# Kernel optimization log

Measured on AMD Instinct MI355X. Metric: run time of the kernel, lower is better.

## Reference

```python
import jax, jax.numpy as jnp
import numpy as np

KSZ = 3      # kernel_size
NH = 4       # num_heads


def setup_inputs() -> dict:
    key = jax.random.key(0)
    ks = jax.random.split(key, 4)
    B, D, H, W, C = 1, 28, 28, 28, 192
    N = D * H * W
    s = 0.02  # trunc_normal std used by the module's init
    return {
        "x": jax.random.normal(ks[0], (B, N, C), jnp.float32),
        "Wq": jax.random.normal(ks[1], (C, C), jnp.float32) * s,
        "bq": jnp.zeros((C,), jnp.float32),
        "Wkv": jax.random.normal(ks[2], (C, 2 * C), jnp.float32) * s,
        "bkv": jnp.zeros((2 * C,), jnp.float32),
        "Wp": jax.random.normal(ks[3], (C, C), jnp.float32) * s,
        "bp": jnp.zeros((C,), jnp.float32),
        "D": D, "H": H, "W": W,
    }


def _windows(t, D, H, W):
    # t: (B, D+2, H+2, W+2, nh, hc) zero-padded; gather the 27 neighborhood
    # offsets (same flattening order as unfold: d-major, then h, then w).
    return jnp.stack(
        [t[:, dz:dz + D, dy:dy + H, dx:dx + W]
         for dz in range(KSZ) for dy in range(KSZ) for dx in range(KSZ)],
        axis=4)  # (B, D, H, W, 27, nh, hc)


def reference(x, Wq, bq, Wkv, bkv, Wp, bp, D, H, W):
    B, N, C = x.shape
    hc = C // NH
    scale = hc ** (-0.5)
    xv = x.reshape(B, D, H, W, C)

    q = (xv @ Wq + bq).reshape(B, D, H, W, NH, hc) * scale
    kv = (xv @ Wkv + bkv).reshape(B, D, H, W, 2, NH, hc)
    k, v = kv[..., 0, :, :], kv[..., 1, :, :]

    pad = ((0, 0), (1, 1), (1, 1), (1, 1), (0, 0), (0, 0))
    kwin = _windows(jnp.pad(k, pad), D, H, W)  # (B,D,H,W,27,nh,hc)
    vwin = _windows(jnp.pad(v, pad), D, H, W)

    # per-voxel 1x27 attention over the 3x3x3 neighborhood
    attn = jnp.einsum('bdhwnc,bdhwknc->bdhwnk', q, kwin)
    attn = jax.nn.softmax(attn, axis=-1)
    out = jnp.einsum('bdhwnk,bdhwknc->bdhwnc', attn, vwin)
    out = out.reshape(B, D, H, W, C) @ Wp + bp
    return out.reshape(B, N, C)
```

## Files before the change

kernel.cpp:

```cpp
#include <hip/hip_runtime.h>
#include <hip/hip_bf16.h>
#include <math.h>

#define CDIM 192
#define DD 28
#define NVOX (DD * DD * DD)
#define NLINE (DD * DD)
#define LSTRIDE (24 * DD * 8)

typedef __attribute__((ext_vector_type(8))) short bf16x8;
typedef __attribute__((ext_vector_type(4))) float f32x4;

__device__ __forceinline__ float blo(unsigned int u) {
  union { unsigned int i; float f; } w; w.i = u << 16; return w.f;
}
__device__ __forceinline__ float bhi(unsigned int u) {
  union { unsigned int i; float f; } w; w.i = u & 0xffff0000u; return w.f;
}
__device__ __forceinline__ unsigned short f2bf(float f) {
  union { float ff; unsigned int i; } w; w.ff = f;
  unsigned int x = w.i;
  return (unsigned short)((x + 0x7fffu + ((x >> 16) & 1u)) >> 16);
}
__device__ __forceinline__ unsigned int pk2(float lo, float hi) {
  __hip_bfloat162 h = __float22bfloat162_rn(make_float2(lo, hi));
  union { __hip_bfloat162 h2; unsigned int u; } cv; cv.h2 = h; return cv.u;
}

__global__ __launch_bounds__(256) void prep_w(
    const float* __restrict__ Wq, const float* __restrict__ Wkv,
    const float* __restrict__ Wp, const float* __restrict__ bq,
    const float* __restrict__ bkv,
    unsigned short* __restrict__ WqkvT, unsigned short* __restrict__ WpT,
    float* __restrict__ biasAll, float scale)
{
  int t = blockIdx.x * 256 + threadIdx.x;
  if (t < 576 * CDIM) {
    const int n = t / CDIM, k = t % CDIM;
    const float v = (n < CDIM) ? Wq[k * CDIM + n] * scale
                               : Wkv[k * 2 * CDIM + (n - CDIM)];
    WqkvT[t] = f2bf(v);
    return;
  }
  t -= 576 * CDIM;
  if (t < CDIM * CDIM) {
    const int n = t / CDIM, k = t % CDIM;
    WpT[t] = f2bf(Wp[k * CDIM + n]);
    return;
  }
  t -= CDIM * CDIM;
  if (t < 576)
    biasAll[t] = (t < CDIM) ? bq[t] * scale : bkv[t - CDIM];
}

__global__ __launch_bounds__(256) void gemm_qkv(
    const float* __restrict__ X,
    const unsigned short* __restrict__ Bt,
    const float* __restrict__ biasAll,
    unsigned short* __restrict__ qb,
    unsigned short* __restrict__ kxb,
    unsigned short* __restrict__ vxb)
{
  __shared__ unsigned short As[64 * 200];
  __shared__ unsigned short Bs[64 * 200];
  const int tid = threadIdx.x;
  const int m0 = blockIdx.x * 64;
  const int by = blockIdx.y;

#pragma unroll
  for (int u = tid; u < 1536; u += 256) {
    const int row = u / 24, c = (u % 24) * 8;
    const float4 f0 = *(const float4*)(&X[(size_t)(m0 + row) * CDIM + c]);
    const float4 f1 = *(const float4*)(&X[(size_t)(m0 + row) * CDIM + c + 4]);
    unsigned int o[4] = {pk2(f0.x, f0.y), pk2(f0.z, f0.w),
                         pk2(f1.x, f1.y), pk2(f1.z, f1.w)};
    *(uint4*)(&As[row * 200 + c]) = *(const uint4*)o;
  }

  const int l = tid & 63, w = tid >> 6;
  const int wm = (w >> 1) * 32, wn = (w & 1) * 32;
  const int lr = l & 15, lk = (l >> 4) * 8;
  const unsigned short* pa = &As[(wm + lr) * 200 + lk];
  const unsigned short* pb = &Bs[(wn + lr) * 200 + lk];

  for (int nt = by; nt < 9; nt += 3) {
    const int n0 = nt * 64;
    __syncthreads();
#pragma unroll
    for (int u = tid; u < 1536; u += 256) {
      const int row = u / 24, c = (u % 24) * 8;
      *(uint4*)(&Bs[row * 200 + c]) =
          *(const uint4*)(&Bt[(size_t)(n0 + row) * CDIM + c]);
    }
    __syncthreads();

    f32x4 acc[2][2] = {};
#pragma unroll
    for (int k0 = 0; k0 < CDIM; k0 += 32) {
      const bf16x8 a0 = *(const bf16x8*)(pa + k0);
      const bf16x8 a1 = *(const bf16x8*)(pa + 16 * 200 + k0);
      const bf16x8 b0 = *(const bf16x8*)(pb + k0);
      const bf16x8 b1 = *(const bf16x8*)(pb + 16 * 200 + k0);
      acc[0][0] = __builtin_amdgcn_mfma_f32_16x16x32_bf16(a0, b0, acc[0][0], 0, 0, 0);
      acc[0][1] = __builtin_amdgcn_mfma_f32_16x16x32_bf16(a0, b1, acc[0][1], 0, 0, 0);
      acc[1][0] = __builtin_amdgcn_mfma_f32_16x16x32_bf16(a1, b0, acc[1][0], 0, 0, 0);
      acc[1][1] = __builtin_amdgcn_mfma_f32_16x16x32_bf16(a1, b1, acc[1][1], 0, 0, 0);
    }

#pragma unroll
    for (int i = 0; i < 2; ++i)
#pragma unroll
      for (int j = 0; j < 2; ++j) {
        const int gc = n0 + wn + j * 16 + lr;
        const float bv = biasAll[gc];
#pragma unroll
        for (int r = 0; r < 4; ++r) {
          const int gr = m0 + wm + i * 16 + (l >> 4) * 4 + r;
          const float v = acc[i][j][r] + bv;
          const unsigned short bfv = f2bf(v);
          if (gc < CDIM) {
            qb[(size_t)gr * CDIM + gc] = bfv;
          } else {
            const int cc = (gc < 2 * CDIM) ? gc - CDIM : gc - 2 * CDIM;
            const int zy = gr / DD, xx = gr - zy * DD;
            const int dst = zy * LSTRIDE + (cc >> 3) * (DD * 8) + xx * 8 + (cc & 7);
            if (gc < 2 * CDIM) kxb[dst] = bfv;
            else               vxb[dst] = bfv;
          }
        }
      }
  }
}

__global__ __launch_bounds__(256, 3) void attn3d_proj(
    const unsigned short* __restrict__ q,
    const unsigned short* __restrict__ kx,
    const unsigned short* __restrict__ vx,
    const unsigned short* __restrict__ WpT,
    const float* __restrict__ bp,
    float* __restrict__ C)
{
  __shared__ unsigned short ytile[32 * 200];

  const int bid = blockIdx.x;
  const int zy = (bid & 7) * 98 + (bid >> 3);
  const int z = zy / 28, yr = zy % 28;
  const int h = threadIdx.x >> 6;
  const int lane = threadIdx.x & 63;
  const int x = lane & 31;
  const int xc = x < 28 ? x : 27;
  const int g = lane >> 5;
  const int cb = h * 48 + g * 24;
  const int cgb = h * 6 + g * 3;
  const int vox = zy * 28 + xc;

  if (threadIdx.x < 100)
    *(uint4*)(&ytile[28 * 200 + threadIdx.x * 8]) = make_uint4(0, 0, 0, 0);

  float qf[24];
  {
    const uint4* qp = (const uint4*)(q + (size_t)vox * CDIM + cb);
    const uint4 a = qp[0], b = qp[1], c = qp[2];
    const unsigned int uu[12] = {a.x, a.y, a.z, a.w, b.x, b.y, b.z, b.w,
                                 c.x, c.y, c.z, c.w};
#pragma unroll
    for (int i = 0; i < 12; ++i) { qf[2*i] = blo(uu[i]); qf[2*i+1] = bhi(uu[i]); }
  }

  const int nx = 3 - (x == 0) - (x == 27);
  const int ny = 3 - (yr == 0) - (yr == 27);
  const int nz = 3 - (z == 0) - (z == 27);
  const int noob = 27 - nx * ny * nz;
  float m = noob ? 0.f : -INFINITY;
  float s = (float)noob;
  float out[24];
#pragma unroll
  for (int i = 0; i < 24; ++i) out[i] = 0.f;

  const bool okm = (x > 0), okp = (x < 27);
  const int xm = okm ? xc - 1 : 0;
  const int xp = okp ? xc + 1 : 27;

  int offm[3], offc[3], offp[3];
#pragma unroll
  for (int i = 0; i < 3; ++i) {
    const int ub = (cgb + i) * (DD * 8);
    offm[i] = ub + xm * 8; offc[i] = ub + xc * 8; offp[i] = ub + xp * 8;
  }

  for (int dz = -1; dz <= 1; ++dz) {
    const int zz = z + dz;
    if ((unsigned)zz >= 28u) continue;
    for (int dy = -1; dy <= 1; ++dy) {
      const int yv = yr + dy;
      if ((unsigned)yv >= 28u) continue;
      const size_t lbase = (size_t)(zz * 28 + yv) * LSTRIDE;
      const unsigned short* kl = kx + lbase;
      const unsigned short* vl = vx + lbase;

      const uint4 Km0 = *(const uint4*)(kl + offm[0]);
      const uint4 Km1 = *(const uint4*)(kl + offm[1]);
      const uint4 Km2 = *(const uint4*)(kl + offm[2]);
      const uint4 Kc0 = *(const uint4*)(kl + offc[0]);
      const uint4 Kc1 = *(const uint4*)(kl + offc[1]);
      const uint4 Kc2 = *(const uint4*)(kl + offc[2]);
      const uint4 Kp0 = *(const uint4*)(kl + offp[0]);
      const uint4 Kp1 = *(const uint4*)(kl + offp[1]);
      const uint4 Kp2 = *(const uint4*)(kl + offp[2]);
      const unsigned int km[12] = {Km0.x, Km0.y, Km0.z, Km0.w, Km1.x, Km1.y,
                                   Km1.z, Km1.w, Km2.x, Km2.y, Km2.z, Km2.w};
      const unsigned int kc[12] = {Kc0.x, Kc0.y, Kc0.z, Kc0.w, Kc1.x, Kc1.y,
                                   Kc1.z, Kc1.w, Kc2.x, Kc2.y, Kc2.z, Kc2.w};
      const unsigned int kp[12] = {Kp0.x, Kp0.y, Kp0.z, Kp0.w, Kp1.x, Kp1.y,
                                   Kp1.z, Kp1.w, Kp2.x, Kp2.y, Kp2.z, Kp2.w};
      float p0 = 0.f, p1 = 0.f, p2 = 0.f;
#pragma unroll
      for (int i = 0; i < 12; ++i) {
        p0 += qf[2*i] * blo(km[i]) + qf[2*i+1] * bhi(km[i]);
        p1 += qf[2*i] * blo(kc[i]) + qf[2*i+1] * bhi(kc[i]);
        p2 += qf[2*i] * blo(kp[i]) + qf[2*i+1] * bhi(kp[i]);
      }
      p0 += __shfl_xor(p0, 32);
      p1 += __shfl_xor(p1, 32);
      p2 += __shfl_xor(p2, 32);

      const uint4 Vm0 = *(const uint4*)(vl + offm[0]);
      const uint4 Vm1 = *(const uint4*)(vl + offm[1]);
      const uint4 Vm2 = *(const uint4*)(vl + offm[2]);
      const uint4 Vc0 = *(const uint4*)(vl + offc[0]);
      const uint4 Vc1 = *(const uint4*)(vl + offc[1]);
      const uint4 Vc2 = *(const uint4*)(vl + offc[2]);
      const uint4 Vp0 = *(const uint4*)(vl + offp[0]);
      const uint4 Vp1 = *(const uint4*)(vl + offp[1]);
      const uint4 Vp2 = *(const uint4*)(vl + offp[2]);

      const float l0 = okm ? p0 : -INFINITY;
      const float l2 = okp ? p2 : -INFINITY;
      const float nm = fmaxf(m, fmaxf(p1, fmaxf(l0, l2)));
      const float sc = __expf(m - nm);
      const float w0 = okm ? __expf(p0 - nm) : 0.f;
      const float w1 = __expf(p1 - nm);
      const float w2 = okp ? __expf(p2 - nm) : 0.f;
      s = s * sc + w0 + w1 + w2;
      m = nm;

      const unsigned int vm[12] = {Vm0.x, Vm0.y, Vm0.z, Vm0.w, Vm1.x, Vm1.y,
                                   Vm1.z, Vm1.w, Vm2.x, Vm2.y, Vm2.z, Vm2.w};
      const unsigned int vc[12] = {Vc0.x, Vc0.y, Vc0.z, Vc0.w, Vc1.x, Vc1.y,
                                   Vc1.z, Vc1.w, Vc2.x, Vc2.y, Vc2.z, Vc2.w};
      const unsigned int vp[12] = {Vp0.x, Vp0.y, Vp0.z, Vp0.w, Vp1.x, Vp1.y,
                                   Vp1.z, Vp1.w, Vp2.x, Vp2.y, Vp2.z, Vp2.w};
#pragma unroll
      for (int i = 0; i < 12; ++i) {
        out[2*i]   = out[2*i]   * sc + w0 * blo(vm[i]) + w1 * blo(vc[i]) + w2 * blo(vp[i]);
        out[2*i+1] = out[2*i+1] * sc + w0 * bhi(vm[i]) + w1 * bhi(vc[i]) + w2 * bhi(vp[i]);
      }
    }
  }

  if (x < 28) {
    const float inv = 1.f / s;
    unsigned int ou[12];
#pragma unroll
    for (int i = 0; i < 12; ++i)
      ou[i] = pk2(out[2*i] * inv, out[2*i+1] * inv);
    uint4* yp = (uint4*)(&ytile[xc * 200 + cb]);
    yp[0] = make_uint4(ou[0], ou[1], ou[2], ou[3]);
    yp[1] = make_uint4(ou[4], ou[5], ou[6], ou[7]);
    yp[2] = make_uint4(ou[8], ou[9], ou[10], ou[11]);
  }
  __syncthreads();

  const int w = threadIdx.x >> 6;
  const int lr = lane & 15, lk = (lane >> 4) * 8;
  const int nb = w * 48;

  f32x4 acc[2][3] = {};
#pragma unroll
  for (int k0 = 0; k0 < CDIM; k0 += 32) {
    const bf16x8 a0 = *(const bf16x8*)(&ytile[(0 + lr) * 200 + lk + k0]);
    const bf16x8 a1 = *(const bf16x8*)(&ytile[(16 + lr) * 200 + lk + k0]);
#pragma unroll
    for (int nj = 0; nj < 3; ++nj) {
      const bf16x8 b = *(const bf16x8*)(
          &WpT[(size_t)(nb + nj * 16 + lr) * CDIM + lk + k0]);
      acc[0][nj] = __builtin_amdgcn_mfma_f32_16x16x32_bf16(a0, b, acc[0][nj], 0, 0, 0);
      acc[1][nj] = __builtin_amdgcn_mfma_f32_16x16x32_bf16(a1, b, acc[1][nj], 0, 0, 0);
    }
  }

#pragma unroll
  for (int nj = 0; nj < 3; ++nj) {
    const int gc = nb + nj * 16 + lr;
    const float bv = bp[gc];
#pragma unroll
    for (int mi = 0; mi < 2; ++mi)
#pragma unroll
      for (int r = 0; r < 4; ++r) {
        const int row = mi * 16 + (lane >> 4) * 4 + r;
        if (row < 28)
          C[(size_t)(zy * 28 + row) * CDIM + gc] = acc[mi][nj][r] + bv;
      }
  }
}

extern "C" void kernel_launch(void* const* d_in, const int* in_sizes, int n_in,
                              void* d_out, int out_size, void* d_ws, size_t ws_size,
                              hipStream_t stream) {
  const float* x   = (const float*)d_in[0];
  const float* Wq  = (const float*)d_in[1];
  const float* bq  = (const float*)d_in[2];
  const float* Wkv = (const float*)d_in[3];
  const float* bkv = (const float*)d_in[4];
  const float* Wp  = (const float*)d_in[5];
  const float* bp  = (const float*)d_in[6];
  float* out = (float*)d_out;

  unsigned short* WqkvT = (unsigned short*)d_ws;
  unsigned short* WpT   = WqkvT + 576 * CDIM;
  float*          biasA = (float*)(WpT + CDIM * CDIM);
  unsigned short* qb    = (unsigned short*)(biasA + 576);
  unsigned short* kxb   = qb + (size_t)NVOX * CDIM;
  unsigned short* vxb   = kxb + (size_t)NLINE * LSTRIDE;

  const float scale = 1.0f / sqrtf(48.0f);

  prep_w<<<(148032 + 255) / 256, 256, 0, stream>>>(
      Wq, Wkv, Wp, bq, bkv, WqkvT, WpT, biasA, scale);

  gemm_qkv<<<dim3(NVOX / 64, 3), 256, 0, stream>>>(x, WqkvT, biasA, qb, kxb, vxb);
  attn3d_proj<<<NLINE, 256, 0, stream>>>(qb, kxb, vxb, WpT, bp, out);
}
```

Before: 144.6 us.

## Pre-pack weights into MFMA fragment order and compute QKV per line

Weights are pre-packed so each lane's MFMA B-fragment is one contiguous 16-byte global load, with no shared-memory staging of B. The QKV GEMM now runs one block per 28-voxel line that computes all 576 output columns, reading X once instead of once per column group. The projection in the attention kernel uses the same packed layout. Per-wave register pressure rises (18 accumulators), and 28-row tiles leave part of each MFMA padded with zero rows.

Measured after the change: 136.5 us. 1.06x faster.

```diff
diff --git a/kernel.cpp b/kernel.cpp
--- a/kernel.cpp
+++ b/kernel.cpp
@@ -7,6 +7,8 @@
 #define NVOX (DD * DD * DD)
 #define NLINE (DD * DD)
 #define LSTRIDE (24 * DD * 8)
+#define LSTR 208
+#define SCALE 0.14433756729740643f
 
 typedef __attribute__((ext_vector_type(8))) short bf16x8;
 typedef __attribute__((ext_vector_type(4))) float f32x4;
@@ -27,105 +29,99 @@
   union { __hip_bfloat162 h2; unsigned int u; } cv; cv.h2 = h; return cv.u;
 }
 
-__global__ __launch_bounds__(256) void prep_w(
-    const float* __restrict__ Wq, const float* __restrict__ Wkv,
-    const float* __restrict__ Wp, const float* __restrict__ bq,
-    const float* __restrict__ bkv,
-    unsigned short* __restrict__ WqkvT, unsigned short* __restrict__ WpT,
-    float* __restrict__ biasAll, float scale)
+__global__ __launch_bounds__(256) void prep_pack(
+    const float* __restrict__ Wq, const float* __restrict__ bq,
+    const float* __restrict__ Wkv, const float* __restrict__ bkv,
+    const float* __restrict__ Wp,
+    unsigned short* __restrict__ wpack,
+    unsigned short* __restrict__ ppack,
+    float* __restrict__ biasA)
 {
   int t = blockIdx.x * 256 + threadIdx.x;
-  if (t < 576 * CDIM) {
-    const int n = t / CDIM, k = t % CDIM;
-    const float v = (n < CDIM) ? Wq[k * CDIM + n] * scale
+  if (t < 110592) {
+    const int e = t & 7, ln = (t >> 3) & 63;
+    const int ks = (t >> 9) % 6, ng = (t >> 9) / 6;
+    const int n = ng * 16 + (ln & 15);
+    const int k = ks * 32 + (ln >> 4) * 8 + e;
+    const float v = (n < CDIM) ? Wq[k * CDIM + n] * SCALE
                                : Wkv[k * 2 * CDIM + (n - CDIM)];
-    WqkvT[t] = f2bf(v);
-    return;
-  }
-  t -= 576 * CDIM;
-  if (t < CDIM * CDIM) {
-    const int n = t / CDIM, k = t % CDIM;
-    WpT[t] = f2bf(Wp[k * CDIM + n]);
-    return;
-  }
-  t -= CDIM * CDIM;
-  if (t < 576)
-    biasAll[t] = (t < CDIM) ? bq[t] * scale : bkv[t - CDIM];
-}
-
-__global__ __launch_bounds__(256) void gemm_qkv(
+    wpack[t] = f2bf(v);
+  } else if (t < 147456) {
+    const int u = t - 110592;
+    const int e = u & 7, ln = (u >> 3) & 63;
+    const int ks = (u >> 9) % 6, ng = (u >> 9) / 6;
+    const int n = ng * 16 + (ln & 15);
+    const int k = ks * 32 + (ln >> 4) * 8 + e;
+    ppack[u] = f2bf(Wp[k * CDIM + n]);
+  } else if (t < 148032) {
+    const int u = t - 147456;
+    biasA[u] = (u < CDIM) ? bq[u] * SCALE : bkv[u - CDIM];
+  }
+}
+
+__global__ __launch_bounds__(256, 4) void qkv_line(
     const float* __restrict__ X,
-    const unsigned short* __restrict__ Bt,
-    const float* __restrict__ biasAll,
+    const unsigned short* __restrict__ wpack,
+    const float* __restrict__ biasA,
     unsigned short* __restrict__ qb,
     unsigned short* __restrict__ kxb,
     unsigned short* __restrict__ vxb)
 {
-  __shared__ unsigned short As[64 * 200];
-  __shared__ unsigned short Bs[64 * 200];
+  __shared__ __align__(16) unsigned short As[32 * LSTR];
   const int tid = threadIdx.x;
-  const int m0 = blockIdx.x * 64;
-  const int by = blockIdx.y;
-
-#pragma unroll
-  for (int u = tid; u < 1536; u += 256) {
+  const int zy = blockIdx.x;
+
+  for (int u = tid; u < 672; u += 256) {
     const int row = u / 24, c = (u % 24) * 8;
-    const float4 f0 = *(const float4*)(&X[(size_t)(m0 + row) * CDIM + c]);
-    const float4 f1 = *(const float4*)(&X[(size_t)(m0 + row) * CDIM + c + 4]);
+    const float4 f0 = *(const float4*)(&X[(size_t)(zy * 28 + row) * CDIM + c]);
+    const float4 f1 = *(const float4*)(&X[(size_t)(zy * 28 + row) * CDIM + c + 4]);
     unsigned int o[4] = {pk2(f0.x, f0.y), pk2(f0.z, f0.w),
                          pk2(f1.x, f1.y), pk2(f1.z, f1.w)};
-    *(uint4*)(&As[row * 200 + c]) = *(const uint4*)o;
-  }
-
-  const int l = tid & 63, w = tid >> 6;
-  const int wm = (w >> 1) * 32, wn = (w & 1) * 32;
-  const int lr = l & 15, lk = (l >> 4) * 8;
-  const unsigned short* pa = &As[(wm + lr) * 200 + lk];
-  const unsigned short* pb = &Bs[(wn + lr) * 200 + lk];
-
-  for (int nt = by; nt < 9; nt += 3) {
-    const int n0 = nt * 64;
-    __syncthreads();
-#pragma unroll
-    for (int u = tid; u < 1536; u += 256) {
-      const int row = u / 24, c = (u % 24) * 8;
-      *(uint4*)(&Bs[row * 200 + c]) =
-          *(const uint4*)(&Bt[(size_t)(n0 + row) * CDIM + c]);
+    *(uint4*)(&As[row * LSTR + c]) = *(const uint4*)o;
+  }
+  for (int u = tid; u < 104; u += 256) {
+    const int row = 28 + u / 26, c = (u % 26) * 8;
+    *(uint4*)(&As[row * LSTR + c]) = make_uint4(0, 0, 0, 0);
+  }
+  __syncthreads();
+
+  const int w = tid >> 6;
+  const int lane = tid & 63;
+  const int lr = lane & 15, lk = (lane >> 4) * 8;
+
+  f32x4 acc[2][9] = {};
+#pragma unroll
+  for (int ks = 0; ks < 6; ++ks) {
+    const bf16x8 a0 = *(const bf16x8*)(&As[lr * LSTR + ks * 32 + lk]);
+    const bf16x8 a1 = *(const bf16x8*)(&As[(16 + lr) * LSTR + ks * 32 + lk]);
+#pragma unroll
+    for (int j = 0; j < 9; ++j) {
+      const int ng = w * 9 + j;
+      const bf16x8 b = *(const bf16x8*)(&wpack[((ng * 6 + ks) * 64 + lane) * 8]);
+      acc[0][j] = __builtin_amdgcn_mfma_f32_16x16x32_bf16(a0, b, acc[0][j], 0, 0, 0);
+      acc[1][j] = __builtin_amdgcn_mfma_f32_16x16x32_bf16(a1, b, acc[1][j], 0, 0, 0);
     }
-    __syncthreads();
-
-    f32x4 acc[2][2] = {};
-#pragma unroll
-    for (int k0 = 0; k0 < CDIM; k0 += 32) {
-      const bf16x8 a0 = *(const bf16x8*)(pa + k0);
-      const bf16x8 a1 = *(const bf16x8*)(pa + 16 * 200 + k0);
-      const bf16x8 b0 = *(const bf16x8*)(pb + k0);
-      const bf16x8 b1 = *(const bf16x8*)(pb + 16 * 200 + k0);
-      acc[0][0] = __builtin_amdgcn_mfma_f32_16x16x32_bf16(a0, b0, acc[0][0], 0, 0, 0);
-      acc[0][1] = __builtin_amdgcn_mfma_f32_16x16x32_bf16(a0, b1, acc[0][1], 0, 0, 0);
-      acc[1][0] = __builtin_amdgcn_mfma_f32_16x16x32_bf16(a1, b0, acc[1][0], 0, 0, 0);
-      acc[1][1] = __builtin_amdgcn_mfma_f32_16x16x32_bf16(a1, b1, acc[1][1], 0, 0, 0);
-    }
-
-#pragma unroll
-    for (int i = 0; i < 2; ++i)
-#pragma unroll
-      for (int j = 0; j < 2; ++j) {
-        const int gc = n0 + wn + j * 16 + lr;
-        const float bv = biasAll[gc];
-#pragma unroll
-        for (int r = 0; r < 4; ++r) {
-          const int gr = m0 + wm + i * 16 + (l >> 4) * 4 + r;
-          const float v = acc[i][j][r] + bv;
-          const unsigned short bfv = f2bf(v);
-          if (gc < CDIM) {
-            qb[(size_t)gr * CDIM + gc] = bfv;
+  }
+
+#pragma unroll
+  for (int j = 0; j < 9; ++j) {
+    const int n = (w * 9 + j) * 16 + lr;
+    const float bv = biasA[n];
+#pragma unroll
+    for (int mi = 0; mi < 2; ++mi)
+#pragma unroll
+      for (int rr = 0; rr < 4; ++rr) {
+        const int row = mi * 16 + (lane >> 4) * 4 + rr;
+        if (row < 28) {
+          const unsigned short bfv = f2bf(acc[mi][j][rr] + bv);
+          if (n < CDIM) {
+            qb[(size_t)(zy * 28 + row) * CDIM + n] = bfv;
           } else {
-            const int cc = (gc < 2 * CDIM) ? gc - CDIM : gc - 2 * CDIM;
-            const int zy = gr / DD, xx = gr - zy * DD;
-            const int dst = zy * LSTRIDE + (cc >> 3) * (DD * 8) + xx * 8 + (cc & 7);
-            if (gc < 2 * CDIM) kxb[dst] = bfv;
-            else               vxb[dst] = bfv;
+            const int c = n - CDIM;
+            const int cc = (c < CDIM) ? c : c - CDIM;
+            const int dst = zy * LSTRIDE + (cc >> 3) * (DD * 8) + row * 8 + (cc & 7);
+            if (c < CDIM) kxb[dst] = bfv;
+            else          vxb[dst] = bfv;
           }
         }
       }
@@ -136,11 +132,11 @@
     const unsigned short* __restrict__ q,
     const unsigned short* __restrict__ kx,
     const unsigned short* __restrict__ vx,
-    const unsigned short* __restrict__ WpT,
+    const unsigned short* __restrict__ ppack,
     const float* __restrict__ bp,
     float* __restrict__ C)
 {
-  __shared__ unsigned short ytile[32 * 200];
+  __shared__ __align__(16) unsigned short ytile[32 * 200];
 
   const int bid = blockIdx.x;
   const int zy = (bid & 7) * 98 + (bid >> 3);
@@ -180,7 +176,6 @@
   const bool okm = (x > 0), okp = (x < 27);
   const int xm = okm ? xc - 1 : 0;
   const int xp = okp ? xc + 1 : 27;
-
   int offm[3], offc[3], offp[3];
 #pragma unroll
   for (int i = 0; i < 3; ++i) {
@@ -273,33 +268,31 @@
 
   const int w = threadIdx.x >> 6;
   const int lr = lane & 15, lk = (lane >> 4) * 8;
-  const int nb = w * 48;
 
   f32x4 acc[2][3] = {};
 #pragma unroll
-  for (int k0 = 0; k0 < CDIM; k0 += 32) {
-    const bf16x8 a0 = *(const bf16x8*)(&ytile[(0 + lr) * 200 + lk + k0]);
-    const bf16x8 a1 = *(const bf16x8*)(&ytile[(16 + lr) * 200 + lk + k0]);
+  for (int ks = 0; ks < 6; ++ks) {
+    const bf16x8 a0 = *(const bf16x8*)(&ytile[lr * 200 + ks * 32 + lk]);
+    const bf16x8 a1 = *(const bf16x8*)(&ytile[(16 + lr) * 200 + ks * 32 + lk]);
 #pragma unroll
     for (int nj = 0; nj < 3; ++nj) {
-      const bf16x8 b = *(const bf16x8*)(
-          &WpT[(size_t)(nb + nj * 16 + lr) * CDIM + lk + k0]);
+      const int ngp = w * 3 + nj;
+      const bf16x8 b = *(const bf16x8*)(&ppack[((ngp * 6 + ks) * 64 + lane) * 8]);
       acc[0][nj] = __builtin_amdgcn_mfma_f32_16x16x32_bf16(a0, b, acc[0][nj], 0, 0, 0);
       acc[1][nj] = __builtin_amdgcn_mfma_f32_16x16x32_bf16(a1, b, acc[1][nj], 0, 0, 0);
     }
   }
-
 #pragma unroll
   for (int nj = 0; nj < 3; ++nj) {
-    const int gc = nb + nj * 16 + lr;
+    const int gc = w * 48 + nj * 16 + lr;
     const float bv = bp[gc];
 #pragma unroll
     for (int mi = 0; mi < 2; ++mi)
 #pragma unroll
-      for (int r = 0; r < 4; ++r) {
-        const int row = mi * 16 + (lane >> 4) * 4 + r;
+      for (int rr = 0; rr < 4; ++rr) {
+        const int row = mi * 16 + (lane >> 4) * 4 + rr;
         if (row < 28)
-          C[(size_t)(zy * 28 + row) * CDIM + gc] = acc[mi][nj][r] + bv;
+          C[(size_t)(zy * 28 + row) * CDIM + gc] = acc[mi][nj][rr] + bv;
       }
   }
 }
@@ -316,18 +309,14 @@
   const float* bp  = (const float*)d_in[6];
   float* out = (float*)d_out;
 
-  unsigned short* WqkvT = (unsigned short*)d_ws;
-  unsigned short* WpT   = WqkvT + 576 * CDIM;
-  float*          biasA = (float*)(WpT + CDIM * CDIM);
+  unsigned short* wpack = (unsigned short*)d_ws;
+  unsigned short* ppack = wpack + 110592;
+  float*          biasA = (float*)(ppack + 36864);
   unsigned short* qb    = (unsigned short*)(biasA + 576);
   unsigned short* kxb   = qb + (size_t)NVOX * CDIM;
   unsigned short* vxb   = kxb + (size_t)NLINE * LSTRIDE;
 
-  const float scale = 1.0f / sqrtf(48.0f);
-
-  prep_w<<<(148032 + 255) / 256, 256, 0, stream>>>(
-      Wq, Wkv, Wp, bq, bkv, WqkvT, WpT, biasA, scale);
-
-  gemm_qkv<<<dim3(NVOX / 64, 3), 256, 0, stream>>>(x, WqkvT, biasA, qb, kxb, vxb);
-  attn3d_proj<<<NLINE, 256, 0, stream>>>(qb, kxb, vxb, WpT, bp, out);
-}
+  prep_pack<<<579, 256, 0, stream>>>(Wq, bq, Wkv, bkv, Wp, wpack, ppack, biasA);
+  qkv_line<<<NLINE, 256, 0, stream>>>(x, wpack, biasA, qb, kxb, vxb);
+  attn3d_proj<<<NLINE, 256, 0, stream>>>(qb, kxb, vxb, ppack, bp, out);
+}
```
